# Kernel optimization log

Hardware: AMD Instinct MI355X
Metric: run time of the kernel (lower is better)

## Reference

```python
import jax, jax.numpy as jnp
import numpy as np

N = 786432   # total points (batch of ~4 LiDAR scans)
U = 131072   # occupied voxels
FEA_DIM = 9
EPS = 1e-5


def _bn_params(key, c):
    k1, k2, k3, k4 = jax.random.split(key, 4)
    g = 1.0 + 0.1 * jax.random.normal(k1, (c,), jnp.float32)
    b = 0.1 * jax.random.normal(k2, (c,), jnp.float32)
    m = 0.1 * jax.random.normal(k3, (c,), jnp.float32)
    v = jax.random.uniform(k4, (c,), jnp.float32, 0.5, 1.5)
    return jnp.stack([g, b, m, v])  # [4, c]


def _linear(key, fin, fout):
    kw, kb = jax.random.split(key)
    w = jax.random.normal(kw, (fin, fout), jnp.float32) / np.sqrt(fin)
    b = 0.01 * jax.random.normal(kb, (fout,), jnp.float32)
    return w, b


def setup_inputs() -> dict:
    key = jax.random.key(0)
    ks = jax.random.split(key, 12)
    cat_pt_fea = jax.random.normal(ks[0], (N, FEA_DIM), jnp.float32)
    occupy = (jax.random.uniform(ks[1], (N, 1)) < 0.9).astype(jnp.float32)
    # voxel coords [batch_idx, 3 cyl inds]; values arbitrary ints (metadata only)
    unq = jax.random.randint(ks[2], (U, 4), 0, 480, dtype=jnp.int32)
    # inverse map point->voxel, guaranteeing every voxel is hit at least once
    unq_inv = jnp.concatenate([
        jnp.arange(U, dtype=jnp.int32),
        jax.random.randint(ks[3], (N - U,), 0, U, dtype=jnp.int32)])
    bn0 = _bn_params(ks[4], FEA_DIM)
    w1, b1 = _linear(ks[5], FEA_DIM, 64)
    bn2 = _bn_params(ks[6], 64)
    w2, b2 = _linear(ks[7], 64, 128)
    bn5 = _bn_params(ks[8], 128)
    w3, b3 = _linear(ks[9], 128, 256)
    bn8 = _bn_params(ks[10], 256)
    w4, b4 = _linear(jax.random.fold_in(key, 100), 256, 256)
    wc, bc = _linear(ks[11], 256, 16)
    return dict(cat_pt_fea=cat_pt_fea, occupy=occupy, unq=unq, unq_inv=unq_inv,
                bn0=bn0, w1=w1, b1=b1, bn2=bn2, w2=w2, b2=b2, bn5=bn5,
                w3=w3, b3=b3, bn8=bn8, w4=w4, b4=b4, wc=wc, bc=bc)


def _bn(x, p):
    g, b, m, v = p[0], p[1], p[2], p[3]
    return (x - m) * (g * jax.lax.rsqrt(v + EPS)) + b


def reference(cat_pt_fea, occupy, unq, unq_inv, bn0, w1, b1, bn2, w2, b2,
              bn5, w3, b3, bn8, w4, b4, wc, bc):
    # per-point PointNet MLP with occupy masking after BN/Linear layers
    x = _bn(cat_pt_fea, bn0) * occupy
    x = (x @ w1 + b1) * occupy
    x = _bn(x, bn2) * occupy
    x = jax.nn.relu(x)
    x = (x @ w2 + b2) * occupy
    x = _bn(x, bn5) * occupy
    x = jax.nn.relu(x)
    x = (x @ w3 + b3) * occupy
    x = _bn(x, bn8) * occupy
    x = jax.nn.relu(x)
    x = (x @ w4 + b4) * occupy                       # [N, 256]
    num_vox = unq.shape[0]
    pooled = jax.ops.segment_max(x, unq_inv, num_segments=num_vox)  # [U, 256]
    # occupy of the max-index point per voxel (mirrors scatter_max on arange)
    unq_idx = jax.ops.segment_max(jnp.arange(unq_inv.shape[0]), unq_inv,
                                  num_segments=num_vox)
    pooled_occupy = occupy[unq_idx]                  # [U, 1]
    out = jax.nn.relu(pooled @ wc + bc) * pooled_occupy  # fea_compression
    return unq, out, pooled_occupy
```

## Files before the change

### kernel.cpp

```cpp
#include <hip/hip_runtime.h>

#define N_PTS 786432
#define U_VOX 131072
#define NBLK  (N_PTS/64)

typedef __attribute__((ext_vector_type(8))) short v8s;
typedef __attribute__((ext_vector_type(4))) float v4f;

__device__ __forceinline__ unsigned short f2bf(float x){
    unsigned u = __float_as_uint(x);
    u += 0x7fffu + ((u >> 16) & 1u);
    return (unsigned short)(u >> 16);
}
__device__ __forceinline__ unsigned cvtpk(float lo, float hi){
    unsigned r;
    asm("v_cvt_pk_bf16_f32 %0, %1, %2" : "=v"(r) : "v"(lo), "v"(hi));
    return r;
}

__global__ __launch_bounds__(256) void k_fold(
    const float* __restrict__ bn0, const float* __restrict__ w1,
    const float* __restrict__ b1,  const float* __restrict__ bn2,
    const float* __restrict__ w2,  const float* __restrict__ b2,
    const float* __restrict__ bn5, const float* __restrict__ w3,
    const float* __restrict__ b3,  const float* __restrict__ bn8,
    const float* __restrict__ w4,  const float* __restrict__ wc,
    float* __restrict__ b1ff, float* __restrict__ b2f, float* __restrict__ b3f,
    unsigned short* __restrict__ wp1, unsigned short* __restrict__ wp2,
    unsigned short* __restrict__ wp3, unsigned short* __restrict__ wp4,
    unsigned short* __restrict__ wcp)
{
    __shared__ float s0[9],t0[9],s2[64],t2[64],s5[128],t5[128],s8[256],t8[256];
    int tid = threadIdx.x;
    if (tid < 9){  float g=bn0[tid], b=bn0[9+tid],  m=bn0[18+tid],  v=bn0[27+tid];
        float s=g*rsqrtf(v+1e-5f); s0[tid]=s; t0[tid]=b-m*s; }
    if (tid < 64){ float g=bn2[tid], b=bn2[64+tid], m=bn2[128+tid], v=bn2[192+tid];
        float s=g*rsqrtf(v+1e-5f); s2[tid]=s; t2[tid]=b-m*s; }
    if (tid < 128){float g=bn5[tid], b=bn5[128+tid],m=bn5[256+tid], v=bn5[384+tid];
        float s=g*rsqrtf(v+1e-5f); s5[tid]=s; t5[tid]=b-m*s; }
    { float g=bn8[tid], b=bn8[256+tid], m=bn8[512+tid], v=bn8[768+tid];
        float s=g*rsqrtf(v+1e-5f); s8[tid]=s; t8[tid]=b-m*s; }
    __syncthreads();
    if (blockIdx.x == 0){
        if (tid < 64){ float a=0.f;
            for (int k=0;k<9;k++) a += t0[k]*w1[k*64+tid];
            b1ff[tid]=(a+b1[tid])*s2[tid]+t2[tid]; }
        if (tid<128) b2f[tid]=b2[tid]*s5[tid]+t5[tid];
        b3f[tid]=b3[tid]*s8[tid]+t8[tid];
    }
    const int g0 = blockIdx.x*256 + tid, gstep = 32*256;
    for (int e=g0;e<2048;e+=gstep){
        int i=e&7, l=(e>>3)&63, jt=(e>>9)&3;
        int k=((l>>4)<<3)+i, j=jt*16+(l&15);
        wp1[e] = (k<9) ? f2bf(s0[k]*w1[k*64+j]*s2[j]) : (unsigned short)0;
    }
    for (int e=g0;e<8192;e+=gstep){
        int i=e&7, l=(e>>3)&63, jt=(e>>9)&7, ks=(e>>12)&1;
        int k=ks*32+((l>>4)<<3)+i, j=jt*16+(l&15);
        wp2[e]=f2bf(w2[k*128+j]*s5[j]);
    }
    for (int e=g0;e<32768;e+=gstep){
        int i=e&7, l=(e>>3)&63, jt=(e>>9)&15, ks=e>>13;
        int k=ks*32+((l>>4)<<3)+i, j=jt*16+(l&15);
        wp3[e]=f2bf(w3[k*256+j]*s8[j]);
    }
    for (int e=g0;e<65536;e+=gstep){
        int i=e&7, l=(e>>3)&63, jt=(e>>9)&15, ks=e>>13;
        int k=ks*32+((l>>4)<<3)+i, j=jt*16+(l&15);
        wp4[e]=f2bf(w4[k*256+j]);
    }
    for (int e=g0;e<4096;e+=gstep){
        int i=e&7, l=(e>>3)&63, ks=e>>9;
        int k=ks*32+((l>>4)<<3)+i, j=l&15;
        wcp[e]=f2bf(wc[k*16+j]);
    }
}

__global__ void k_hist(const int* __restrict__ uinv, int* __restrict__ cnt){
    int i=blockIdx.x*256+threadIdx.x;
    atomicAdd(cnt + uinv[i], 1);
}
__global__ void k_scan1(int* __restrict__ cnt, int* __restrict__ bsum){
    __shared__ int s[256];
    int t=threadIdx.x, i=blockIdx.x*256+t;
    int v=cnt[i]; s[t]=v; __syncthreads();
    for (int off=1;off<256;off<<=1){
        int x=(t>=off)?s[t-off]:0; __syncthreads();
        s[t]+=x; __syncthreads();
    }
    cnt[i]=s[t]-v;
    if (t==255) bsum[blockIdx.x]=s[255];
}
__global__ void k_scan2(int* __restrict__ bsum){
    __shared__ int s[512];
    int t=threadIdx.x;
    int v=bsum[t]; s[t]=v; __syncthreads();
    for (int off=1;off<512;off<<=1){
        int x=(t>=off)?s[t-off]:0; __syncthreads();
        s[t]+=x; __syncthreads();
    }
    bsum[t]=s[t]-v;
}
__global__ void k_scan3(const int* __restrict__ cnt, const int* __restrict__ bsum,
                        int* __restrict__ cur){
    int i=blockIdx.x*256+threadIdx.x;
    cur[i]=cnt[i]+bsum[blockIdx.x];
}
__global__ void k_scatgath(const int* __restrict__ uinv,
    const float* __restrict__ cat, const float* __restrict__ occ,
    int* __restrict__ cur, int* __restrict__ uidx,
    unsigned short* __restrict__ scat16, int* __restrict__ svoxS)
{
    int i = blockIdx.x*256 + threadIdx.x;
    int v = uinv[i];
    int slot = atomicAdd(cur + v, 1);
    atomicMax(uidx + v, i);
    const float* src = cat + (size_t)i*9;
    unsigned short tmp[16];
#pragma unroll
    for (int k=0;k<9;k++) tmp[k] = f2bf(src[k]);
    tmp[9] = f2bf(occ[i]);
#pragma unroll
    for (int k=10;k<16;k++) tmp[k]=0;
    uint4* dst = (uint4*)(scat16 + (size_t)slot*16);
    dst[0] = *(uint4*)(tmp);
    dst[1] = *(uint4*)(tmp+8);
    svoxS[slot] = v;
}

__global__ __launch_bounds__(256,4) void k_fused(
    const unsigned short* __restrict__ scat16g, const int* __restrict__ svoxS,
    const unsigned short* __restrict__ wp1, const float* __restrict__ b1ff,
    const unsigned short* __restrict__ wp2, const float* __restrict__ b2f,
    const unsigned short* __restrict__ wp3, const float* __restrict__ b3f,
    const unsigned short* __restrict__ wp4, const float* __restrict__ b4,
    unsigned* __restrict__ pooled, unsigned* __restrict__ bpool)
{
    __shared__ __align__(16) char smem[34320];
    int*   svox = (int*)smem;
    float* socc = (float*)(smem+256);
    int*   vpn  = (int*)(smem+512);
    float* pmlo = (float*)(smem+528);
    float* pmhi = (float*)(smem+1040);
    char*  R1   = smem + 1552;
    char*  sh1  = R1 + 4096;
    char*  sh2  = R1 + 12288;

    const int tid = threadIdx.x;
    const int blk = blockIdx.x;
    const int p0  = blk*64;
    const int w = tid>>6, l = tid&63, lane16 = l&15, hi = l>>4;

    if (tid < 128){
        uint4 d = *(const uint4*)(scat16g + (size_t)p0*16 + tid*8);
        int p = tid>>1, q = tid&1;
        *(uint4*)(R1 + p*64 + ((q*16) ^ ((p&3)<<4))) = d;
    } else {
        int t2 = tid-128; int p = t2>>1, q = t2&1;
        *(uint4*)(R1 + p*64 + ((32 + q*16) ^ ((p&3)<<4))) = make_uint4(0,0,0,0);
    }
    if (tid < 64) svox[tid] = svoxS[p0 + tid];
    if (tid == 64) vpn[0] = (p0>0) ? svoxS[p0-1] : -1;
    if (tid == 65) vpn[1] = (p0+64<N_PTS) ? svoxS[p0+64] : -1;
    __syncthreads();
    if (tid < 64){
        unsigned short ob = *(unsigned short*)(R1 + tid*64 + (18 ^ ((tid&3)<<4)));
        socc[tid] = __uint_as_float(((unsigned)ob)<<16);
    }

    {
        v4f bias = *(const v4f*)(b1ff + w*16 + 4*hi);
        v8s aw = *(const v8s*)(wp1 + (size_t)(w*64 + l)*8);
        v4f acc1[4];
#pragma unroll
        for (int mt=0;mt<4;mt++){
            int P = mt*16 + lane16;
            v8s act = *(const v8s*)(R1 + P*64 + ((hi*16) ^ ((P&3)<<4)));
            acc1[mt] = __builtin_amdgcn_mfma_f32_16x16x32_bf16(aw, act, bias, 0,0,0);
        }
#pragma unroll
        for (int mt=0;mt<4;mt++){
            int P = mt*16 + lane16, key = (P&7)<<4;
            int cb = (w*16 + 4*hi)*2;
            float v0=fmaxf(acc1[mt][0],0.f), v1=fmaxf(acc1[mt][1],0.f);
            float v2=fmaxf(acc1[mt][2],0.f), v3=fmaxf(acc1[mt][3],0.f);
            *(unsigned*)(sh1 + P*128 + ((cb  )^key)) = cvtpk(v0,v1);
            *(unsigned*)(sh1 + P*128 + ((cb+4)^key)) = cvtpk(v2,v3);
        }
    }
    __syncthreads();

    {
        v4f acc2[4][2];
#pragma unroll
        for (int jj=0;jj<2;jj++){
            v4f bias = *(const v4f*)(b2f + w*32 + jj*16 + 4*hi);
#pragma unroll
            for (int mt=0;mt<4;mt++) acc2[mt][jj]=bias;
        }
#pragma unroll
        for (int ks=0;ks<2;ks++){
            v8s a[4];
#pragma unroll
            for (int mt=0;mt<4;mt++){
                int P = mt*16 + lane16;
                a[mt] = *(const v8s*)(sh1 + P*128 + ((ks*64 + hi*16) ^ ((P&7)<<4)));
            }
#pragma unroll
            for (int jj=0;jj<2;jj++){
                v8s bw = *(const v8s*)(wp2 + (size_t)((ks*8 + w*2 + jj)*64 + l)*8);
#pragma unroll
                for (int mt=0;mt<4;mt++)
                    acc2[mt][jj]=__builtin_amdgcn_mfma_f32_16x16x32_bf16(bw, a[mt], acc2[mt][jj],0,0,0);
            }
        }
#pragma unroll
        for (int mt=0;mt<4;mt++){
            int P = mt*16 + lane16, key = (P&7)<<4;
#pragma unroll
            for (int jj=0;jj<2;jj++){
                int cb = (w*32 + jj*16 + 4*hi)*2;
                float v0=fmaxf(acc2[mt][jj][0],0.f), v1=fmaxf(acc2[mt][jj][1],0.f);
                float v2=fmaxf(acc2[mt][jj][2],0.f), v3=fmaxf(acc2[mt][jj][3],0.f);
                *(unsigned*)(sh2 + P*256 + ((cb  )^key)) = cvtpk(v0,v1);
                *(unsigned*)(sh2 + P*256 + ((cb+4)^key)) = cvtpk(v2,v3);
            }
        }
    }
    __syncthreads();

    {
        v4f acc3[4][4];
#pragma unroll
        for (int jj=0;jj<4;jj++){
            v4f bias = *(const v4f*)(b3f + w*64 + jj*16 + 4*hi);
#pragma unroll
            for (int mt=0;mt<4;mt++) acc3[mt][jj]=bias;
        }
#pragma unroll
        for (int ks=0;ks<4;ks++){
            v8s a[4];
#pragma unroll
            for (int mt=0;mt<4;mt++){
                int P = mt*16 + lane16;
                a[mt] = *(const v8s*)(sh2 + P*256 + ((ks*64 + hi*16) ^ ((P&7)<<4)));
            }
#pragma unroll
            for (int jj=0;jj<4;jj++){
                v8s bw = *(const v8s*)(wp3 + (size_t)((ks*16 + w*4 + jj)*64 + l)*8);
#pragma unroll
                for (int mt=0;mt<4;mt++)
                    acc3[mt][jj]=__builtin_amdgcn_mfma_f32_16x16x32_bf16(bw, a[mt], acc3[mt][jj],0,0,0);
            }
        }
        __syncthreads();
#pragma unroll
        for (int mt=0;mt<4;mt++){
            int P = mt*16 + lane16, key = (P&7)<<4;
#pragma unroll
            for (int jj=0;jj<4;jj++){
                int cb = (w*64 + jj*16 + 4*hi)*2;
                float v0=fmaxf(acc3[mt][jj][0],0.f), v1=fmaxf(acc3[mt][jj][1],0.f);
                float v2=fmaxf(acc3[mt][jj][2],0.f), v3=fmaxf(acc3[mt][jj][3],0.f);
                *(unsigned*)(R1 + P*512 + ((cb  )^key)) = cvtpk(v0,v1);
                *(unsigned*)(R1 + P*512 + ((cb+4)^key)) = cvtpk(v2,v3);
            }
        }
    }
    __syncthreads();

    {
        v4f acc4[4][4];
#pragma unroll
        for (int jj=0;jj<4;jj++){
            v4f bias = *(const v4f*)(b4 + w*64 + jj*16 + 4*hi);
#pragma unroll
            for (int mt=0;mt<4;mt++) acc4[mt][jj]=bias;
        }
#pragma unroll
        for (int ks=0;ks<8;ks++){
            v8s a[4];
#pragma unroll
            for (int mt=0;mt<4;mt++){
                int P = mt*16 + lane16;
                a[mt] = *(const v8s*)(R1 + P*512 + ((ks*64 + hi*16) ^ ((P&7)<<4)));
            }
#pragma unroll
            for (int jj=0;jj<4;jj++){
                v8s bw = *(const v8s*)(wp4 + (size_t)((ks*16 + w*4 + jj)*64 + l)*8);
#pragma unroll
                for (int mt=0;mt<4;mt++)
                    acc4[mt][jj]=__builtin_amdgcn_mfma_f32_16x16x32_bf16(bw, a[mt], acc4[mt][jj],0,0,0);
            }
        }
        __syncthreads();
#pragma unroll
        for (int mt=0;mt<4;mt++){
            int P = mt*16 + lane16, key = (P&7)<<4;
            float oc = socc[P];
#pragma unroll
            for (int jj=0;jj<4;jj++){
                int cb = (w*64 + jj*16 + 4*hi)*2;
                *(unsigned*)(R1 + P*512 + ((cb  )^key)) = cvtpk(acc4[mt][jj][0]*oc, acc4[mt][jj][1]*oc);
                *(unsigned*)(R1 + P*512 + ((cb+4)^key)) = cvtpk(acc4[mt][jj][2]*oc, acc4[mt][jj][3]*oc);
            }
        }
    }
    __syncthreads();

    {
        const int half = tid>>7, c = tid&127, rb = half*32;
        int vl = svox[l];
        int vln = (l<63)? svox[l+1] : (int)0x80000000;
        unsigned long long mask = __ballot((l==63) || (vl!=vln));
        const int vp0=vpn[0], vp1=vpn[1];
        const bool cross = (svox[31]==svox[32]);
        float m0=-3.0e38f, m1=-3.0e38f, d0=0.f, d1=0.f;
        int segStart = rb, dEnd = 0; bool defer=false;
#pragma unroll 8
        for (int k=0;k<32;k++){
            int r = rb + k;
            unsigned x = *(const unsigned*)(R1 + r*512 + ((c*4) ^ ((k&7)<<4)));
            m0 = fmaxf(m0, __uint_as_float(x<<16));
            m1 = fmaxf(m1, __uint_as_float(x & 0xFFFF0000u));
            if ((mask>>r)&1ull){
                int v = svox[r];
                if (half==1 && segStart==32 && cross){
                    defer=true; d0=m0; d1=m1; dEnd=r;
                } else {
                    bool bp = (segStart==0) && (v==vp0);
                    bool bn = (r==63) && (v==vp1);
                    unsigned pk = cvtpk(m0,m1);
                    if (bp) bpool[((size_t)blk*2+0)*128 + c] = pk;
                    if (bn) bpool[((size_t)blk*2+1)*128 + c] = pk;
                    if (!bp && !bn) pooled[(size_t)v*128 + c] = pk;
                }
                m0=-3.0e38f; m1=-3.0e38f; segStart=r+1;
            }
        }
        if (half==0 && !((mask>>31)&1ull)){ pmlo[c]=m0; pmhi[c]=m1; }
        __syncthreads();
        if (defer){
            m0 = fmaxf(d0, pmlo[c]); m1 = fmaxf(d1, pmhi[c]);
            unsigned long long lowm = mask & 0x7FFFFFFFull;
            int ts = lowm ? (64 - __clzll(lowm)) : 0;
            int v = svox[32];
            bool bp = (ts==0) && (v==vp0);
            bool bn = (dEnd==63) && (v==vp1);
            unsigned pk = cvtpk(m0,m1);
            if (bp) bpool[((size_t)blk*2+0)*128 + c] = pk;
            if (bn) bpool[((size_t)blk*2+1)*128 + c] = pk;
            if (!bp && !bn) pooled[(size_t)v*128 + c] = pk;
        }
    }
}

__global__ __launch_bounds__(256) void k_bmerge(
    const int* __restrict__ cnt, const int* __restrict__ bsum,
    const int* __restrict__ cur, const unsigned* __restrict__ bpool,
    unsigned* __restrict__ pooled)
{
    int tid = threadIdx.x;
    int c = tid & 127, vv = tid>>7;
    int base = blockIdx.x*16 + vv*8;
#pragma unroll
    for (int i=0;i<8;i++){
        int v = base + i;
        int start = cnt[v] + bsum[v>>8];
        int end   = cur[v];
        int bs = start>>6, be = (end-1)>>6;
        if (bs==be) continue;
        unsigned x = bpool[((size_t)bs*2+1)*128 + c];
        float m0 = __uint_as_float(x<<16);
        float m1 = __uint_as_float(x & 0xFFFF0000u);
        for (int b=bs+1;b<be;b++){
            unsigned y = bpool[((size_t)b*2+1)*128 + c];
            m0 = fmaxf(m0, __uint_as_float(y<<16));
            m1 = fmaxf(m1, __uint_as_float(y & 0xFFFF0000u));
        }
        unsigned z = bpool[((size_t)be*2+0)*128 + c];
        m0 = fmaxf(m0, __uint_as_float(z<<16));
        m1 = fmaxf(m1, __uint_as_float(z & 0xFFFF0000u));
        pooled[(size_t)v*128 + c] = cvtpk(m0,m1);
    }
}

__global__ __launch_bounds__(256) void k_head(
    const unsigned short* __restrict__ pooled16,
    const unsigned short* __restrict__ wcp, const float* __restrict__ bc,
    const float* __restrict__ occ, const int* __restrict__ uidx,
    float* __restrict__ outf)
{
    __shared__ float pocc[64];
    int tid=threadIdx.x;
    int v0 = blockIdx.x*64;
    if (tid<64){
        float p = occ[uidx[v0+tid]];
        pocc[tid]=p;
        outf[2621440 + v0 + tid] = p;
    }
    __syncthreads();
    int w=tid>>6, l=tid&63, lane16=l&15, hi=l>>4;
    int vb = w*16;
    float bcj = bc[lane16];
    v4f acc = {bcj,bcj,bcj,bcj};
#pragma unroll
    for (int ks=0;ks<8;ks++){
        v8s a = *(const v8s*)(pooled16 + (size_t)(v0 + vb + lane16)*256 + ks*32 + hi*8);
        v8s b = *(const v8s*)(wcp + (size_t)(ks*64 + l)*8);
        acc = __builtin_amdgcn_mfma_f32_16x16x32_bf16(a, b, acc, 0,0,0);
    }
#pragma unroll
    for (int r=0;r<4;r++){
        int vx = vb + 4*hi + r;
        outf[524288 + (size_t)(v0+vx)*16 + lane16] = fmaxf(acc[r],0.f) * pocc[vx];
    }
}

__global__ void k_unq(const int* __restrict__ unq, float* __restrict__ o){
    int i=blockIdx.x*256+threadIdx.x;
    o[i]=(float)unq[i];
}

extern "C" void kernel_launch(void* const* d_in, const int* in_sizes, int n_in,
                              void* d_out, int out_size, void* d_ws, size_t ws_size,
                              hipStream_t stream)
{
    const float* cat =(const float*)d_in[0];
    const float* occ =(const float*)d_in[1];
    const int*   unq =(const int*)  d_in[2];
    const int*   uinv=(const int*)  d_in[3];
    const float* bn0 =(const float*)d_in[4];
    const float* w1  =(const float*)d_in[5];
    const float* b1  =(const float*)d_in[6];
    const float* bn2 =(const float*)d_in[7];
    const float* w2  =(const float*)d_in[8];
    const float* b2  =(const float*)d_in[9];
    const float* bn5 =(const float*)d_in[10];
    const float* w3  =(const float*)d_in[11];
    const float* b3  =(const float*)d_in[12];
    const float* bn8 =(const float*)d_in[13];
    const float* w4  =(const float*)d_in[14];
    const float* b4  =(const float*)d_in[15];
    const float* wc  =(const float*)d_in[16];
    const float* bc  =(const float*)d_in[17];

    unsigned* pooled = (unsigned*)d_ws;
    unsigned short* scat16 = (unsigned short*)((char*)d_ws + (size_t)U_VOX*128*4);
    int* svoxS = (int*)(scat16 + (size_t)N_PTS*16);
    unsigned* bpool = (unsigned*)(svoxS + N_PTS);

    float* outf = (float*)d_out;
    int*   uidx = (int*)d_out;
    float* b1ff = outf + 131072;
    float* b2f  = b1ff + 64;
    float* b3f  = b2f + 128;
    unsigned short* wp1 = (unsigned short*)(outf + 131520);
    unsigned short* wp2 = (unsigned short*)(outf + 132544);
    unsigned short* wp3 = (unsigned short*)(outf + 136640);
    unsigned short* wp4 = (unsigned short*)(outf + 153024);
    unsigned short* wcp = (unsigned short*)(outf + 185792);
    int* cnt  = (int*)(outf + 187840);
    int* cur  = (int*)(outf + 318912);
    int* bsum = (int*)(outf + 449984);

    hipMemsetAsync((void*)uidx, 0, (size_t)U_VOX*4, stream);
    hipMemsetAsync((void*)cnt,  0, (size_t)U_VOX*4, stream);
    k_fold    <<<32,        256,0,stream>>>(bn0,w1,b1,bn2,w2,b2,bn5,w3,b3,bn8,w4,wc,
                                            b1ff,b2f,b3f,wp1,wp2,wp3,wp4,wcp);
    k_hist    <<<N_PTS/256, 256,0,stream>>>(uinv,cnt);
    k_scan1   <<<U_VOX/256, 256,0,stream>>>(cnt,bsum);
    k_scan2   <<<1,         512,0,stream>>>(bsum);
    k_scan3   <<<U_VOX/256, 256,0,stream>>>(cnt,bsum,cur);
    k_scatgath<<<N_PTS/256, 256,0,stream>>>(uinv,cat,occ,cur,uidx,scat16,svoxS);
    k_fused   <<<NBLK,      256,0,stream>>>(scat16,svoxS,wp1,b1ff,wp2,b2f,
                                            wp3,b3f,wp4,b4,pooled,bpool);
    k_bmerge  <<<U_VOX/16,  256,0,stream>>>(cnt,bsum,cur,bpool,pooled);
    k_head    <<<U_VOX/64,  256,0,stream>>>((unsigned short*)pooled,wcp,bc,occ,uidx,outf);
    k_unq     <<<U_VOX*4/256,256,0,stream>>>(unq,outf);
}
```

Before: 331.6 us.

## Replace XOR-swizzled LDS tiles with padded rows and load layer-1 activations directly

The fused MLP kernel drops the XOR-swizzled shared-memory layout in favour of padded row strides (144/272/528 bytes) to avoid bank conflicts with simpler addressing. Layer-1 activations are now read straight from global memory instead of being staged through LDS, which removes the first sync and zero-fill. The unq-to-float conversion is folded into the scan3 kernel, saving one launch. Scratch buffers move from the output buffer into the workspace, so the two memsets become one. The padding adds about 1 KB of LDS per block, which may affect occupancy.

Result: slower. 343.8 us (+3.7%).

```diff
diff --git a/kernel.cpp b/kernel.cpp
--- a/kernel.cpp
+++ b/kernel.cpp
@@ -101,10 +101,13 @@
     }
     bsum[t]=s[t]-v;
 }
-__global__ void k_scan3(const int* __restrict__ cnt, const int* __restrict__ bsum,
-                        int* __restrict__ cur){
+__global__ void k_scan3u(const int* __restrict__ cnt, const int* __restrict__ bsum,
+                         int* __restrict__ cur,
+                         const int* __restrict__ unq, float* __restrict__ outf){
     int i=blockIdx.x*256+threadIdx.x;
     cur[i]=cnt[i]+bsum[blockIdx.x];
+    int4 u = *(const int4*)(unq + 4*i);
+    *(float4*)(outf + 4*i) = make_float4((float)u.x,(float)u.y,(float)u.z,(float)u.w);
 }
 __global__ void k_scatgath(const int* __restrict__ uinv,
     const float* __restrict__ cat, const float* __restrict__ occ,
@@ -136,173 +139,149 @@
     const unsigned short* __restrict__ wp4, const float* __restrict__ b4,
     unsigned* __restrict__ pooled, unsigned* __restrict__ bpool)
 {
-    __shared__ __align__(16) char smem[34320];
+    __shared__ __align__(16) char smem[35344];
     int*   svox = (int*)smem;
     float* socc = (float*)(smem+256);
     int*   vpn  = (int*)(smem+512);
     float* pmlo = (float*)(smem+528);
     float* pmhi = (float*)(smem+1040);
     char*  R1   = smem + 1552;
-    char*  sh1  = R1 + 4096;
-    char*  sh2  = R1 + 12288;
+    char*  sh1  = R1;
+    char*  sh2  = R1 + 9216;
 
     const int tid = threadIdx.x;
     const int blk = blockIdx.x;
     const int p0  = blk*64;
     const int w = tid>>6, l = tid&63, lane16 = l&15, hi = l>>4;
 
-    if (tid < 128){
-        uint4 d = *(const uint4*)(scat16g + (size_t)p0*16 + tid*8);
-        int p = tid>>1, q = tid&1;
-        *(uint4*)(R1 + p*64 + ((q*16) ^ ((p&3)<<4))) = d;
-    } else {
-        int t2 = tid-128; int p = t2>>1, q = t2&1;
-        *(uint4*)(R1 + p*64 + ((32 + q*16) ^ ((p&3)<<4))) = make_uint4(0,0,0,0);
-    }
-    if (tid < 64) svox[tid] = svoxS[p0 + tid];
-    if (tid == 64) vpn[0] = (p0>0) ? svoxS[p0-1] : -1;
-    if (tid == 65) vpn[1] = (p0+64<N_PTS) ? svoxS[p0+64] : -1;
-    __syncthreads();
-    if (tid < 64){
-        unsigned short ob = *(unsigned short*)(R1 + tid*64 + (18 ^ ((tid&3)<<4)));
-        socc[tid] = __uint_as_float(((unsigned)ob)<<16);
-    }
+    if (tid < 64) svox[tid] = svoxS[p0+tid];
+    if (tid >= 64 && tid < 128){
+        int t = tid-64;
+        unsigned short ob = scat16g[(size_t)(p0+t)*16 + 9];
+        socc[t] = __uint_as_float(((unsigned)ob)<<16);
+    }
+    if (tid==128) vpn[0] = (p0>0)        ? svoxS[p0-1]  : -1;
+    if (tid==129) vpn[1] = (p0+64<N_PTS) ? svoxS[p0+64] : -1;
 
     {
         v4f bias = *(const v4f*)(b1ff + w*16 + 4*hi);
         v8s aw = *(const v8s*)(wp1 + (size_t)(w*64 + l)*8);
-        v4f acc1[4];
+        const unsigned short* abase = scat16g + (size_t)p0*16 + hi*8;
+#pragma unroll
+        for (int mt=0;mt<4;mt++){
+            v8s act = *(const v8s*)(abase + (mt*16+lane16)*16);
+            v4f acc1 = __builtin_amdgcn_mfma_f32_16x16x32_bf16(aw, act, bias, 0,0,0);
+            char* dst = sh1 + (mt*16+lane16)*144 + (w*16 + 4*hi)*2;
+            *(unsigned*)(dst  ) = cvtpk(fmaxf(acc1[0],0.f), fmaxf(acc1[1],0.f));
+            *(unsigned*)(dst+4) = cvtpk(fmaxf(acc1[2],0.f), fmaxf(acc1[3],0.f));
+        }
+    }
+    __syncthreads();
+
+    {
+        v4f acc2[4][2];
+#pragma unroll
+        for (int jj=0;jj<2;jj++){
+            v4f bias = *(const v4f*)(b2f + w*32 + jj*16 + 4*hi);
+#pragma unroll
+            for (int mt=0;mt<4;mt++) acc2[mt][jj]=bias;
+        }
+#pragma unroll
+        for (int ks=0;ks<2;ks++){
+            v8s a[4];
+#pragma unroll
+            for (int mt=0;mt<4;mt++)
+                a[mt] = *(const v8s*)(sh1 + (mt*16+lane16)*144 + hi*16 + ks*64);
+#pragma unroll
+            for (int jj=0;jj<2;jj++){
+                v8s bw = *(const v8s*)(wp2 + (size_t)((ks*8 + w*2 + jj)*64 + l)*8);
+#pragma unroll
+                for (int mt=0;mt<4;mt++)
+                    acc2[mt][jj]=__builtin_amdgcn_mfma_f32_16x16x32_bf16(bw, a[mt], acc2[mt][jj],0,0,0);
+            }
+        }
+#pragma unroll
+        for (int mt=0;mt<4;mt++){
+            char* dst = sh2 + (mt*16+lane16)*272;
+#pragma unroll
+            for (int jj=0;jj<2;jj++){
+                int cb = (w*32 + jj*16 + 4*hi)*2;
+                *(unsigned*)(dst+cb  ) = cvtpk(fmaxf(acc2[mt][jj][0],0.f), fmaxf(acc2[mt][jj][1],0.f));
+                *(unsigned*)(dst+cb+4) = cvtpk(fmaxf(acc2[mt][jj][2],0.f), fmaxf(acc2[mt][jj][3],0.f));
+            }
+        }
+    }
+    __syncthreads();
+
+    {
+        v4f acc3[4][4];
+#pragma unroll
+        for (int jj=0;jj<4;jj++){
+            v4f bias = *(const v4f*)(b3f + w*64 + jj*16 + 4*hi);
+#pragma unroll
+            for (int mt=0;mt<4;mt++) acc3[mt][jj]=bias;
+        }
+#pragma unroll
+        for (int ks=0;ks<4;ks++){
+            v8s a[4];
+#pragma unroll
+            for (int mt=0;mt<4;mt++)
+                a[mt] = *(const v8s*)(sh2 + (mt*16+lane16)*272 + hi*16 + ks*64);
+#pragma unroll
+            for (int jj=0;jj<4;jj++){
+                v8s bw = *(const v8s*)(wp3 + (size_t)((ks*16 + w*4 + jj)*64 + l)*8);
+#pragma unroll
+                for (int mt=0;mt<4;mt++)
+                    acc3[mt][jj]=__builtin_amdgcn_mfma_f32_16x16x32_bf16(bw, a[mt], acc3[mt][jj],0,0,0);
+            }
+        }
+        __syncthreads();
+#pragma unroll
+        for (int mt=0;mt<4;mt++){
+            char* dst = R1 + (mt*16+lane16)*528;
+#pragma unroll
+            for (int jj=0;jj<4;jj++){
+                int cb = (w*64 + jj*16 + 4*hi)*2;
+                *(unsigned*)(dst+cb  ) = cvtpk(fmaxf(acc3[mt][jj][0],0.f), fmaxf(acc3[mt][jj][1],0.f));
+                *(unsigned*)(dst+cb+4) = cvtpk(fmaxf(acc3[mt][jj][2],0.f), fmaxf(acc3[mt][jj][3],0.f));
+            }
+        }
+    }
+    __syncthreads();
+
+    {
+        v4f acc4[4][4];
+#pragma unroll
+        for (int jj=0;jj<4;jj++){
+            v4f bias = *(const v4f*)(b4 + w*64 + jj*16 + 4*hi);
+#pragma unroll
+            for (int mt=0;mt<4;mt++) acc4[mt][jj]=bias;
+        }
+#pragma unroll
+        for (int ks=0;ks<8;ks++){
+            v8s a[4];
+#pragma unroll
+            for (int mt=0;mt<4;mt++)
+                a[mt] = *(const v8s*)(R1 + (mt*16+lane16)*528 + hi*16 + ks*64);
+#pragma unroll
+            for (int jj=0;jj<4;jj++){
+                v8s bw = *(const v8s*)(wp4 + (size_t)((ks*16 + w*4 + jj)*64 + l)*8);
+#pragma unroll
+                for (int mt=0;mt<4;mt++)
+                    acc4[mt][jj]=__builtin_amdgcn_mfma_f32_16x16x32_bf16(bw, a[mt], acc4[mt][jj],0,0,0);
+            }
+        }
+        __syncthreads();
 #pragma unroll
         for (int mt=0;mt<4;mt++){
             int P = mt*16 + lane16;
-            v8s act = *(const v8s*)(R1 + P*64 + ((hi*16) ^ ((P&3)<<4)));
-            acc1[mt] = __builtin_amdgcn_mfma_f32_16x16x32_bf16(aw, act, bias, 0,0,0);
-        }
-#pragma unroll
-        for (int mt=0;mt<4;mt++){
-            int P = mt*16 + lane16, key = (P&7)<<4;
-            int cb = (w*16 + 4*hi)*2;
-            float v0=fmaxf(acc1[mt][0],0.f), v1=fmaxf(acc1[mt][1],0.f);
-            float v2=fmaxf(acc1[mt][2],0.f), v3=fmaxf(acc1[mt][3],0.f);
-            *(unsigned*)(sh1 + P*128 + ((cb  )^key)) = cvtpk(v0,v1);
-            *(unsigned*)(sh1 + P*128 + ((cb+4)^key)) = cvtpk(v2,v3);
-        }
-    }
-    __syncthreads();
-
-    {
-        v4f acc2[4][2];
-#pragma unroll
-        for (int jj=0;jj<2;jj++){
-            v4f bias = *(const v4f*)(b2f + w*32 + jj*16 + 4*hi);
-#pragma unroll
-            for (int mt=0;mt<4;mt++) acc2[mt][jj]=bias;
-        }
-#pragma unroll
-        for (int ks=0;ks<2;ks++){
-            v8s a[4];
-#pragma unroll
-            for (int mt=0;mt<4;mt++){
-                int P = mt*16 + lane16;
-                a[mt] = *(const v8s*)(sh1 + P*128 + ((ks*64 + hi*16) ^ ((P&7)<<4)));
-            }
-#pragma unroll
-            for (int jj=0;jj<2;jj++){
-                v8s bw = *(const v8s*)(wp2 + (size_t)((ks*8 + w*2 + jj)*64 + l)*8);
-#pragma unroll
-                for (int mt=0;mt<4;mt++)
-                    acc2[mt][jj]=__builtin_amdgcn_mfma_f32_16x16x32_bf16(bw, a[mt], acc2[mt][jj],0,0,0);
-            }
-        }
-#pragma unroll
-        for (int mt=0;mt<4;mt++){
-            int P = mt*16 + lane16, key = (P&7)<<4;
-#pragma unroll
-            for (int jj=0;jj<2;jj++){
-                int cb = (w*32 + jj*16 + 4*hi)*2;
-                float v0=fmaxf(acc2[mt][jj][0],0.f), v1=fmaxf(acc2[mt][jj][1],0.f);
-                float v2=fmaxf(acc2[mt][jj][2],0.f), v3=fmaxf(acc2[mt][jj][3],0.f);
-                *(unsigned*)(sh2 + P*256 + ((cb  )^key)) = cvtpk(v0,v1);
-                *(unsigned*)(sh2 + P*256 + ((cb+4)^key)) = cvtpk(v2,v3);
-            }
-        }
-    }
-    __syncthreads();
-
-    {
-        v4f acc3[4][4];
-#pragma unroll
-        for (int jj=0;jj<4;jj++){
-            v4f bias = *(const v4f*)(b3f + w*64 + jj*16 + 4*hi);
-#pragma unroll
-            for (int mt=0;mt<4;mt++) acc3[mt][jj]=bias;
-        }
-#pragma unroll
-        for (int ks=0;ks<4;ks++){
-            v8s a[4];
-#pragma unroll
-            for (int mt=0;mt<4;mt++){
-                int P = mt*16 + lane16;
-                a[mt] = *(const v8s*)(sh2 + P*256 + ((ks*64 + hi*16) ^ ((P&7)<<4)));
-            }
-#pragma unroll
-            for (int jj=0;jj<4;jj++){
-                v8s bw = *(const v8s*)(wp3 + (size_t)((ks*16 + w*4 + jj)*64 + l)*8);
-#pragma unroll
-                for (int mt=0;mt<4;mt++)
-                    acc3[mt][jj]=__builtin_amdgcn_mfma_f32_16x16x32_bf16(bw, a[mt], acc3[mt][jj],0,0,0);
-            }
-        }
-        __syncthreads();
-#pragma unroll
-        for (int mt=0;mt<4;mt++){
-            int P = mt*16 + lane16, key = (P&7)<<4;
+            char* dst = R1 + P*528;
+            float oc = socc[P];
 #pragma unroll
             for (int jj=0;jj<4;jj++){
                 int cb = (w*64 + jj*16 + 4*hi)*2;
-                float v0=fmaxf(acc3[mt][jj][0],0.f), v1=fmaxf(acc3[mt][jj][1],0.f);
-                float v2=fmaxf(acc3[mt][jj][2],0.f), v3=fmaxf(acc3[mt][jj][3],0.f);
-                *(unsigned*)(R1 + P*512 + ((cb  )^key)) = cvtpk(v0,v1);
-                *(unsigned*)(R1 + P*512 + ((cb+4)^key)) = cvtpk(v2,v3);
-            }
-        }
-    }
-    __syncthreads();
-
-    {
-        v4f acc4[4][4];
-#pragma unroll
-        for (int jj=0;jj<4;jj++){
-            v4f bias = *(const v4f*)(b4 + w*64 + jj*16 + 4*hi);
-#pragma unroll
-            for (int mt=0;mt<4;mt++) acc4[mt][jj]=bias;
-        }
-#pragma unroll
-        for (int ks=0;ks<8;ks++){
-            v8s a[4];
-#pragma unroll
-            for (int mt=0;mt<4;mt++){
-                int P = mt*16 + lane16;
-                a[mt] = *(const v8s*)(R1 + P*512 + ((ks*64 + hi*16) ^ ((P&7)<<4)));
-            }
-#pragma unroll
-            for (int jj=0;jj<4;jj++){
-                v8s bw = *(const v8s*)(wp4 + (size_t)((ks*16 + w*4 + jj)*64 + l)*8);
-#pragma unroll
-                for (int mt=0;mt<4;mt++)
-                    acc4[mt][jj]=__builtin_amdgcn_mfma_f32_16x16x32_bf16(bw, a[mt], acc4[mt][jj],0,0,0);
-            }
-        }
-        __syncthreads();
-#pragma unroll
-        for (int mt=0;mt<4;mt++){
-            int P = mt*16 + lane16, key = (P&7)<<4;
-            float oc = socc[P];
-#pragma unroll
-            for (int jj=0;jj<4;jj++){
-                int cb = (w*64 + jj*16 + 4*hi)*2;
-                *(unsigned*)(R1 + P*512 + ((cb  )^key)) = cvtpk(acc4[mt][jj][0]*oc, acc4[mt][jj][1]*oc);
-                *(unsigned*)(R1 + P*512 + ((cb+4)^key)) = cvtpk(acc4[mt][jj][2]*oc, acc4[mt][jj][3]*oc);
+                *(unsigned*)(dst+cb  ) = cvtpk(acc4[mt][jj][0]*oc, acc4[mt][jj][1]*oc);
+                *(unsigned*)(dst+cb+4) = cvtpk(acc4[mt][jj][2]*oc, acc4[mt][jj][3]*oc);
             }
         }
     }
@@ -320,7 +299,7 @@
 #pragma unroll 8
         for (int k=0;k<32;k++){
             int r = rb + k;
-            unsigned x = *(const unsigned*)(R1 + r*512 + ((c*4) ^ ((k&7)<<4)));
+            unsigned x = *(const unsigned*)(R1 + r*528 + c*4);
             m0 = fmaxf(m0, __uint_as_float(x<<16));
             m1 = fmaxf(m1, __uint_as_float(x & 0xFFFF0000u));
             if ((mask>>r)&1ull){
@@ -415,11 +394,6 @@
         int vx = vb + 4*hi + r;
         outf[524288 + (size_t)(v0+vx)*16 + lane16] = fmaxf(acc[r],0.f) * pocc[vx];
     }
-}
-
-__global__ void k_unq(const int* __restrict__ unq, float* __restrict__ o){
-    int i=blockIdx.x*256+threadIdx.x;
-    o[i]=(float)unq[i];
 }
 
 extern "C" void kernel_launch(void* const* d_in, const int* in_sizes, int n_in,
@@ -445,37 +419,36 @@
     const float* wc  =(const float*)d_in[16];
     const float* bc  =(const float*)d_in[17];
 
-    unsigned* pooled = (unsigned*)d_ws;
-    unsigned short* scat16 = (unsigned short*)((char*)d_ws + (size_t)U_VOX*128*4);
-    int* svoxS = (int*)(scat16 + (size_t)N_PTS*16);
-    unsigned* bpool = (unsigned*)(svoxS + N_PTS);
+    char* ws = (char*)d_ws;
+    unsigned*       pooled = (unsigned*)ws;
+    unsigned short* scat16 = (unsigned short*)(ws + 67108864);
+    int*            svoxS  = (int*)(ws + 92274688);
+    unsigned*       bpool  = (unsigned*)(ws + 95420416);
+    int*            cnt    = (int*)(ws + 108003328);
+    int*            uidx   = (int*)(ws + 108527616);
+    int*            cur    = (int*)(ws + 109051904);
+    int*            bsum   = (int*)(ws + 109576192);
+    float*          b1ff   = (float*)(ws + 109578240);
+    float*          b2f    = (float*)(ws + 109578496);
+    float*          b3f    = (float*)(ws + 109579008);
+    unsigned short* wp1    = (unsigned short*)(ws + 109580032);
+    unsigned short* wp2    = (unsigned short*)(ws + 109584128);
+    unsigned short* wp3    = (unsigned short*)(ws + 109600512);
+    unsigned short* wp4    = (unsigned short*)(ws + 109666048);
+    unsigned short* wcp    = (unsigned short*)(ws + 109797120);
 
     float* outf = (float*)d_out;
-    int*   uidx = (int*)d_out;
-    float* b1ff = outf + 131072;
-    float* b2f  = b1ff + 64;
-    float* b3f  = b2f + 128;
-    unsigned short* wp1 = (unsigned short*)(outf + 131520);
-    unsigned short* wp2 = (unsigned short*)(outf + 132544);
-    unsigned short* wp3 = (unsigned short*)(outf + 136640);
-    unsigned short* wp4 = (unsigned short*)(outf + 153024);
-    unsigned short* wcp = (unsigned short*)(outf + 185792);
-    int* cnt  = (int*)(outf + 187840);
-    int* cur  = (int*)(outf + 318912);
-    int* bsum = (int*)(outf + 449984);
-
-    hipMemsetAsync((void*)uidx, 0, (size_t)U_VOX*4, stream);
-    hipMemsetAsync((void*)cnt,  0, (size_t)U_VOX*4, stream);
+
+    hipMemsetAsync((void*)cnt, 0, 1048576, stream);
     k_fold    <<<32,        256,0,stream>>>(bn0,w1,b1,bn2,w2,b2,bn5,w3,b3,bn8,w4,wc,
                                             b1ff,b2f,b3f,wp1,wp2,wp3,wp4,wcp);
     k_hist    <<<N_PTS/256, 256,0,stream>>>(uinv,cnt);
     k_scan1   <<<U_VOX/256, 256,0,stream>>>(cnt,bsum);
     k_scan2   <<<1,         512,0,stream>>>(bsum);
-    k_scan3   <<<U_VOX/256, 256,0,stream>>>(cnt,bsum,cur);
+    k_scan3u  <<<U_VOX/256, 256,0,stream>>>(cnt,bsum,cur,unq,outf);
     k_scatgath<<<N_PTS/256, 256,0,stream>>>(uinv,cat,occ,cur,uidx,scat16,svoxS);
     k_fused   <<<NBLK,      256,0,stream>>>(scat16,svoxS,wp1,b1ff,wp2,b2f,
                                             wp3,b3f,wp4,b4,pooled,bpool);
     k_bmerge  <<<U_VOX/16,  256,0,stream>>>(cnt,bsum,cur,bpool,pooled);
     k_head    <<<U_VOX/64,  256,0,stream>>>((unsigned short*)pooled,wcp,bc,occ,uidx,outf);
-    k_unq     <<<U_VOX*4/256,256,0,stream>>>(unq,outf);
-}
+}
```
